# Performance work log

Hardware: AMD Instinct MI355X
Metric: run time of the kernel (lower is better)

Reference implementation:

```python
import jax, jax.numpy as jnp
import numpy as np

OBS_DIM = 4096
NUM_ACTIONS = 18
ACTION_DIM = 64
D_MODEL = 512
N_LAYERS = 4
HIST = 256
BATCH = 32
D_STATE = 16
D_CONV = 4
EXPAND = 2
D_INNER = EXPAND * D_MODEL           # 1024
DT_RANK = -(-D_MODEL // 16)          # ceil(512/16)=32
OBS_OUT = D_MODEL - ACTION_DIM       # 448


def setup_inputs() -> dict:
    key = jax.random.key(0)
    ks = jax.random.split(key, 16)
    s = 0.02
    inp = {
        "obss": jax.random.normal(ks[0], (BATCH, HIST, OBS_DIM), jnp.float32),
        "actions": jax.random.randint(ks[1], (BATCH, HIST, 1), 0, NUM_ACTIONS),
        "obs_W": jax.random.normal(ks[2], (OBS_OUT, OBS_DIM), jnp.float32) * s,
        "obs_b": jnp.zeros((OBS_OUT,), jnp.float32),
        "act_emb": jax.random.normal(ks[3], (NUM_ACTIONS, ACTION_DIM), jnp.float32) * s,
        "pos_emb": jax.random.normal(ks[4], (1, HIST, D_MODEL), jnp.float32) * s,
        # stacked Mamba params, leading dim = N_LAYERS
        "W_in": jax.random.normal(ks[5], (N_LAYERS, 2 * D_INNER, D_MODEL), jnp.float32) * s,
        "conv_w": jax.random.normal(ks[6], (N_LAYERS, D_INNER, D_CONV), jnp.float32) * s,
        "conv_b": jnp.zeros((N_LAYERS, D_INNER), jnp.float32),
        "W_x": jax.random.normal(ks[7], (N_LAYERS, DT_RANK + 2 * D_STATE, D_INNER), jnp.float32) * s,
        "W_dt": jax.random.normal(ks[8], (N_LAYERS, D_INNER, DT_RANK), jnp.float32) * s,
        "b_dt": jnp.full((N_LAYERS, D_INNER), -4.6, jnp.float32),  # softplus(-4.6)~0.01
        "A_log": jnp.log(jnp.broadcast_to(jnp.arange(1, D_STATE + 1, dtype=jnp.float32), (N_LAYERS, D_INNER, D_STATE))),
        "D_p": jnp.ones((N_LAYERS, D_INNER), jnp.float32),
        "W_out": jax.random.normal(ks[9], (N_LAYERS, D_MODEL, D_INNER), jnp.float32) * s,
        "ffn_W1": jax.random.normal(ks[10], (D_MODEL, D_MODEL), jnp.float32) * s,
        "ffn_b1": jnp.zeros((D_MODEL,), jnp.float32),
        "ffn_W2": jax.random.normal(ks[11], (NUM_ACTIONS, D_MODEL), jnp.float32) * s,
        "ffn_b2": jnp.zeros((NUM_ACTIONS,), jnp.float32),
    }
    return inp


def mamba_block(x, W_in, conv_w, conv_b, W_x, W_dt, b_dt, A_log, D_p, W_out):
    # x: (B, L, D_MODEL)
    B_, L, _ = x.shape
    xz = jnp.einsum('bld,ed->ble', x, W_in)            # (B,L,2*Di)
    xi, z = jnp.split(xz, 2, axis=-1)
    # causal depthwise conv1d, kernel D_CONV
    xp = jnp.pad(xi, ((0, 0), (D_CONV - 1, 0), (0, 0)))
    xc = conv_b + sum(conv_w[:, k] * xp[:, k:k + L, :] for k in range(D_CONV))
    xc = jax.nn.silu(xc)                               # (B,L,Di)
    xdbl = jnp.einsum('bld,ed->ble', xc, W_x)          # (B,L,dt_rank+2*ds)
    dt, Bm, Cm = jnp.split(xdbl, [DT_RANK, DT_RANK + D_STATE], axis=-1)
    dt = jax.nn.softplus(jnp.einsum('blr,dr->bld', dt, W_dt) + b_dt)  # (B,L,Di)
    A = -jnp.exp(A_log)                                # (Di,ds)

    def step(h, inp):
        dt_t, B_t, C_t, x_t = inp                      # (B,Di),(B,ds),(B,ds),(B,Di)
        dA = jnp.exp(dt_t[:, :, None] * A)             # (B,Di,ds)
        h = dA * h + dt_t[:, :, None] * B_t[:, None, :] * x_t[:, :, None]
        y = jnp.einsum('bdn,bn->bd', h, C_t)
        return h, y

    h0 = jnp.zeros((B_, D_INNER, D_STATE), xc.dtype)
    xs = (dt.transpose(1, 0, 2), Bm.transpose(1, 0, 2),
          Cm.transpose(1, 0, 2), xc.transpose(1, 0, 2))
    _, ys = jax.lax.scan(step, h0, xs)                 # (L,B,Di)
    y = ys.transpose(1, 0, 2) + xc * D_p
    y = y * jax.nn.silu(z)
    return jnp.einsum('bld,ed->ble', y, W_out)         # (B,L,D_MODEL)


def reference(obss, actions, obs_W, obs_b, act_emb, pos_emb, W_in, conv_w, conv_b,
              W_x, W_dt, b_dt, A_log, D_p, W_out, ffn_W1, ffn_b1, ffn_W2, ffn_b2):
    L = obss.shape[1]
    tok = jnp.einsum('blo,eo->ble', obss, obs_W) + obs_b          # (B,L,448)
    ae = act_emb[actions[:, :, 0]]                                # (B,L,64)
    # torch.roll(ae, 1, 1) with first step zeroed (history_len > 1)
    ae = jnp.concatenate([jnp.zeros_like(ae[:, :1]), ae[:, :-1]], axis=1)
    x = jnp.concatenate([ae, tok], axis=-1) + pos_emb[:, :L, :]   # (B,L,512)
    for i in range(N_LAYERS):
        x = mamba_block(x, W_in[i], conv_w[i], conv_b[i], W_x[i], W_dt[i],
                        b_dt[i], A_log[i], D_p[i], W_out[i])
    h = jax.nn.relu(jnp.einsum('bld,ed->ble', x, ffn_W1) + ffn_b1)
    out = jnp.einsum('bld,ed->ble', h, ffn_W2) + ffn_b2           # (B,L,18)
    return out[:, -L:, :]
```

## Files before the change

### kernel.cpp

```cpp
#include <hip/hip_runtime.h>
#include <hip/hip_bf16.h>
#include <cstdint>
#include <cstddef>

#define HIST    256
#define DMODEL  512
#define DINNER  1024
#define DSTATE  16
#define DTRANK  32
#define OBSDIM  4096
#define OBSOUT  448
#define ADIM    64
#define NLAYERS 4
#define MROWS   8192

typedef __bf16  bf16x8 __attribute__((ext_vector_type(8)));
typedef float   f32x4  __attribute__((ext_vector_type(4)));

enum { MEPI_TOK = 0, MEPI_BF16 = 1, MEPI_SPLIT = 2, MEPI_RELUB = 3, MEPI_PART = 4 };

__device__ __forceinline__ float siluf(float x) { return x / (1.f + __expf(-x)); }
__device__ __forceinline__ float softplusf(float x) {
    return fmaxf(x, 0.f) + log1pf(__expf(-fabsf(x)));
}
__device__ __forceinline__ float bflo(unsigned u) { return __uint_as_float(u << 16); }
__device__ __forceinline__ float bfhi(unsigned u) { return __uint_as_float(u & 0xffff0000u); }

template<int EPI, int NW>
__global__ __launch_bounds__(256)
void gemm_mfma(const __hip_bfloat16* __restrict__ A, int lda,
               const __hip_bfloat16* __restrict__ W,
               float* __restrict__ Cf, int ldc,
               __hip_bfloat16* __restrict__ Cb, int ldcb,
               int coff, int N, int K, int nbn,
               const float* __restrict__ bias, const float* __restrict__ pos)
{
    constexpr int MI   = (NW == 128) ? 4 : 2;
    constexpr int NBUF = (NW == 128) ? 3 : 4;
    __shared__ __hip_bfloat16 Asm[NBUF][128 * 32];
    __shared__ __hip_bfloat16 Bsm[NBUF][NW * 32];
    const int bid = blockIdx.x;
    const int xcd = bid & 7;
    const int s   = bid >> 3;
    int n_blk, m_blk, kc_ = 0;
    if constexpr (EPI == MEPI_PART) {
        m_blk = xcd * 8 + (s >> 2);
        kc_   = s & 3;
        n_blk = 0;
    } else {
        n_blk = s % nbn;
        m_blk = xcd * ((int)(gridDim.x >> 3) / nbn) + s / nbn;
    }
    const int m0 = m_blk * 128;
    const int n0 = n_blk * NW;

    const int tid  = threadIdx.x;
    const int lane = tid & 63;
    const int wv   = tid >> 6;
    const int wm   = (NW == 128) ? ((wv >> 1) << 6) : (wv << 5);
    const int wn   = (NW == 128) ? ((wv & 1) << 6) : 0;
    const int sr   = lane >> 2;
    const int scs  = (((lane & 3) ^ ((lane >> 4) & 3)) << 3);
    const int quad = lane >> 4;
    const int c16  = lane & 15;

    f32x4 acc[MI][4] = {};
    const __hip_bfloat16* aptr = A + (size_t)(m0 + wv * 16 + sr) * lda + scs + kc_ * 256;
    const __hip_bfloat16* bptr = W + (size_t)(n0 + wv * 16 + sr) * K + scs;

#define STAGE(K0, BUF) { \
    __hip_bfloat16* asml = Asm[BUF] + wv * 16 * 32; \
    __hip_bfloat16* bsml = Bsm[BUF] + wv * 16 * 32; \
    __builtin_amdgcn_global_load_lds( \
        (const __attribute__((address_space(1))) void*)(aptr + (K0)), \
        (__attribute__((address_space(3))) void*)(asml), 16, 0, 0); \
    __builtin_amdgcn_global_load_lds( \
        (const __attribute__((address_space(1))) void*)(aptr + (size_t)64 * lda + (K0)), \
        (__attribute__((address_space(3))) void*)(asml + 64 * 32), 16, 0, 0); \
    __builtin_amdgcn_global_load_lds( \
        (const __attribute__((address_space(1))) void*)(bptr + (K0)), \
        (__attribute__((address_space(3))) void*)(bsml), 16, 0, 0); \
    if (NW == 128) \
        __builtin_amdgcn_global_load_lds( \
            (const __attribute__((address_space(1))) void*)(bptr + (size_t)64 * K + (K0)), \
            (__attribute__((address_space(3))) void*)(bsml + 64 * 32), 16, 0, 0); \
    }

    auto kstep = [&](int buf) {
        __builtin_amdgcn_s_barrier();
        __builtin_amdgcn_sched_barrier(0);
        bf16x8 af[MI], bfr[4];
        const int csw = ((quad ^ ((c16 >> 2) & 3)) << 3);
        #pragma unroll
        for (int i = 0; i < MI; ++i)
            af[i]  = *(const bf16x8*)(Asm[buf] + (wm + i * 16 + c16) * 32 + csw);
        #pragma unroll
        for (int j = 0; j < 4; ++j)
            bfr[j] = *(const bf16x8*)(Bsm[buf] + (wn + j * 16 + c16) * 32 + csw);
        #pragma unroll
        for (int i = 0; i < MI; ++i)
            #pragma unroll
            for (int j = 0; j < 4; ++j)
                acc[i][j] = __builtin_amdgcn_mfma_f32_16x16x32_bf16(af[i], bfr[j], acc[i][j], 0, 0, 0);
        __builtin_amdgcn_sched_barrier(0);
        __builtin_amdgcn_s_barrier();
    };

    const int NT = K >> 5;
    #pragma unroll
    for (int t = 0; t < NBUF - 1; ++t) STAGE(t << 5, t)
    int sb = NBUF - 1, cb = 0;
    int it = 0;
    for (; it + NBUF - 1 < NT; ++it) {
        STAGE((it + NBUF - 1) << 5, sb)
        sb = (sb + 1 == NBUF) ? 0 : sb + 1;
        if constexpr (NW == 128) asm volatile("s_waitcnt vmcnt(8)" ::: "memory");
        else                     asm volatile("s_waitcnt vmcnt(9)" ::: "memory");
        kstep(cb);
        cb = (cb + 1 == NBUF) ? 0 : cb + 1;
    }
    if constexpr (NW == 64) {
        asm volatile("s_waitcnt vmcnt(6)" ::: "memory");
        kstep(cb); cb = (cb + 1 == NBUF) ? 0 : cb + 1;
        asm volatile("s_waitcnt vmcnt(3)" ::: "memory");
        kstep(cb); cb = (cb + 1 == NBUF) ? 0 : cb + 1;
        asm volatile("s_waitcnt vmcnt(0)" ::: "memory");
        kstep(cb);
    } else {
        asm volatile("s_waitcnt vmcnt(4)" ::: "memory");
        kstep(cb); cb = (cb + 1 == NBUF) ? 0 : cb + 1;
        asm volatile("s_waitcnt vmcnt(0)" ::: "memory");
        kstep(cb);
    }
#undef STAGE

    #pragma unroll
    for (int i = 0; i < MI; ++i) {
        const int mbase = m0 + wm + i * 16 + quad * 4;
        #pragma unroll
        for (int j = 0; j < 4; ++j) {
            const int n = n0 + wn + j * 16 + c16;
            if (n < N) {
                #pragma unroll
                for (int r = 0; r < 4; ++r) {
                    const size_t m = mbase + r;
                    float v = acc[i][j][r];
                    if (EPI == MEPI_TOK) {
                        v += bias[n] + pos[(m & (HIST - 1)) * DMODEL + coff + n];
                        Cb[m * ldcb + coff + n] = __float2bfloat16(v);
                    } else if (EPI == MEPI_BF16) {
                        Cb[m * ldcb + n] = __float2bfloat16(v);
                    } else if (EPI == MEPI_SPLIT) {
                        if (n < DTRANK) Cf[m * 32 + n] = v;
                        else Cb[(m >> 1) * 64 + (n & 15) * 4 + (m & 1) * 2 + ((n >> 4) & 1)]
                                 = __float2bfloat16(v);
                    } else if (EPI == MEPI_PART) {
                        Cf[((size_t)kc_ * MROWS + m) * 64 + n] = v;
                    } else {
                        Cb[m * ldcb + n] = __float2bfloat16(fmaxf(v + bias[n], 0.f));
                    }
                }
            }
        }
    }
}

__global__ __launch_bounds__(256)
void combine_split_kernel(const float* __restrict__ p, float* __restrict__ xdt,
                          __hip_bfloat16* __restrict__ bcb)
{
    const int idx = blockIdx.x * 256 + threadIdx.x;
    const int m  = idx >> 4;
    const int n4 = (idx & 15) << 2;
    const float4 a = *(const float4*)(p + (size_t)m * 64 + n4);
    const float4 b = *(const float4*)(p + ((size_t)MROWS + m) * 64 + n4);
    const float4 c = *(const float4*)(p + ((size_t)2 * MROWS + m) * 64 + n4);
    const float4 d = *(const float4*)(p + ((size_t)3 * MROWS + m) * 64 + n4);
    const float v[4] = { a.x + b.x + c.x + d.x, a.y + b.y + c.y + d.y,
                         a.z + b.z + c.z + d.z, a.w + b.w + c.w + d.w };
    if (n4 < 32) {
        *(float4*)(xdt + (size_t)m * 32 + n4) = make_float4(v[0], v[1], v[2], v[3]);
    } else {
        #pragma unroll
        for (int j = 0; j < 4; ++j) {
            const int n = n4 + j;
            bcb[(m >> 1) * 64 + (n & 15) * 4 + (m & 1) * 2 + ((n >> 4) & 1)]
                = __float2bfloat16(v[j]);
        }
    }
}

__global__ __launch_bounds__(256)
void gemm_f32_sp(const float* __restrict__ A, int lda,
                 const float* __restrict__ W,
                 __hip_bfloat16* __restrict__ C, int ldc,
                 int N, int K, const float* __restrict__ bias)
{
    __shared__ float As[32][68];
    __shared__ float Ws[32][68];
    const int tid = threadIdx.x;
    const int tx = tid & 15, ty = tid >> 4;
    const int m0 = blockIdx.y * 64;
    const int n0 = blockIdx.x * 64;
    const int lr = tid >> 3;
    const int lc = (tid & 7) << 2;
    float acc[4][4] = {};
    for (int k0 = 0; k0 < K; k0 += 32) {
        const float4 a0 = *(const float4*)(A + (size_t)(m0 + lr) * lda + k0 + lc);
        const float4 a1 = *(const float4*)(A + (size_t)(m0 + lr + 32) * lda + k0 + lc);
        const float4 b0 = *(const float4*)(W + (size_t)(n0 + lr) * K + k0 + lc);
        const float4 b1 = *(const float4*)(W + (size_t)(n0 + lr + 32) * K + k0 + lc);
        __syncthreads();
        As[lc+0][lr] = a0.x; As[lc+1][lr] = a0.y; As[lc+2][lr] = a0.z; As[lc+3][lr] = a0.w;
        As[lc+0][lr+32] = a1.x; As[lc+1][lr+32] = a1.y; As[lc+2][lr+32] = a1.z; As[lc+3][lr+32] = a1.w;
        Ws[lc+0][lr] = b0.x; Ws[lc+1][lr] = b0.y; Ws[lc+2][lr] = b0.z; Ws[lc+3][lr] = b0.w;
        Ws[lc+0][lr+32] = b1.x; Ws[lc+1][lr+32] = b1.y; Ws[lc+2][lr+32] = b1.z; Ws[lc+3][lr+32] = b1.w;
        __syncthreads();
        #pragma unroll
        for (int k = 0; k < 32; ++k) {
            const float4 a4 = *(const float4*)&As[k][ty << 2];
            const float4 b4 = *(const float4*)&Ws[k][tx << 2];
            const float a[4] = {a4.x, a4.y, a4.z, a4.w};
            const float b[4] = {b4.x, b4.y, b4.z, b4.w};
            #pragma unroll
            for (int i = 0; i < 4; ++i)
                #pragma unroll
                for (int j = 0; j < 4; ++j)
                    acc[i][j] = fmaf(a[i], b[j], acc[i][j]);
        }
    }
    const int mb = m0 + (ty << 2);
    const int nb = n0 + (tx << 2);
    #pragma unroll
    for (int i = 0; i < 4; ++i) {
        const size_t m = mb + i;
        #pragma unroll
        for (int j = 0; j < 4; ++j) {
            const int n = nb + j;
            C[m * ldc + n] = __float2bfloat16(softplusf(acc[i][j] + bias[n]));
        }
    }
}

#define NSEG 15
struct CastSegs {
    const float* src[NSEG];
    unsigned long long dstoff[NSEG];
    int blk_start[NSEG + 1];
    int n4[NSEG];
    int shift[NSEG];
    int nrows[NSEG];
};

__global__ __launch_bounds__(256)
void cast_all_kernel(CastSegs cs, char* wsbase)
{
    const int blk = blockIdx.x;
    int s = 0;
    #pragma unroll 1
    while (s < NSEG - 1 && blk >= cs.blk_start[s + 1]) ++s;
    const int i = (blk - cs.blk_start[s]) * 256 + (int)threadIdx.x;
    if (i >= cs.n4[s]) return;
    const int row = i >> cs.shift[s];
    float4 v = make_float4(0.f, 0.f, 0.f, 0.f);
    if (row < cs.nrows[s]) v = ((const float4*)cs.src[s])[i];
    union { __hip_bfloat16 h[4]; short4 sh; } o;
    o.h[0] = __float2bfloat16(v.x); o.h[1] = __float2bfloat16(v.y);
    o.h[2] = __float2bfloat16(v.z); o.h[3] = __float2bfloat16(v.w);
    ((short4*)(wsbase + cs.dstoff[s]))[i] = o.sh;
}

__global__ __launch_bounds__(256)
void embed_kernel(const int* __restrict__ actions, const float* __restrict__ act_emb,
                  const float* __restrict__ pos_emb, __hip_bfloat16* __restrict__ xb)
{
    const int idx = blockIdx.x * 256 + threadIdx.x;
    const int e = idx & 63;
    const int m = idx >> 6;
    const int l = m & (HIST - 1);
    const int b = m >> 8;
    float v = pos_emb[l * DMODEL + e];
    if (l > 0) {
        const int a = actions[b * HIST + l - 1];
        v += act_emb[a * ADIM + e];
    }
    xb[(size_t)m * DMODEL + e] = __float2bfloat16(v);
}

__global__ __launch_bounds__(256)
void conv_silu_kernel(const __hip_bfloat16* __restrict__ xzb, const float* __restrict__ cw,
                      const float* __restrict__ cb, __hip_bfloat16* __restrict__ xcb)
{
    const int idx = blockIdx.x * 256 + threadIdx.x;
    const int d = idx & (DINNER - 1);
    const int m = idx >> 10;
    const int l = m & (HIST - 1);
    const float4 w = ((const float4*)cw)[d];
    const __hip_bfloat16* basep = xzb + (size_t)m * (2 * DINNER) + d;
    float acc = cb[d] + w.w * __bfloat162float(basep[0]);
    if (l >= 1) acc = fmaf(w.z, __bfloat162float(basep[-2 * DINNER]), acc);
    if (l >= 2) acc = fmaf(w.y, __bfloat162float(basep[-4 * DINNER]), acc);
    if (l >= 3) acc = fmaf(w.x, __bfloat162float(basep[-6 * DINNER]), acc);
    xcb[idx] = __float2bfloat16(siluf(acc));
}

#define DPPA(x, CTRL) { float _t; \
    asm("v_add_f32_dpp %0, %1, %1 " CTRL " row_mask:0xf bank_mask:0xf" \
        : "=v"(_t) : "v"(x)); x = _t; }

__global__ __launch_bounds__(256)
void scan_kernel(const __hip_bfloat16* __restrict__ dtb, const __hip_bfloat16* __restrict__ bcb,
                 const __hip_bfloat16* __restrict__ xcb, const __hip_bfloat16* __restrict__ zb,
                 const float* __restrict__ A_log, const float* __restrict__ D_p,
                 __hip_bfloat16* __restrict__ yb)
{
    __shared__ unsigned sdx[2][16][68];
    __shared__ unsigned sbc[2][16][68];

    const int tid = threadIdx.x;
    const int n   = tid & 15;
    const int g   = tid >> 4;

    const int bid = blockIdx.x;
    const int blk = ((bid & 7) << 8) | (bid >> 3);
    const int c0  = blk * 16;
    const int b   = c0 >> 10;
    const int d0  = c0 & (DINNER - 1);
    const int d   = d0 + g;
    const size_t row0 = (size_t)b * HIST;

    const int sr = tid >> 2;
    const int sq = tid & 3;
    const unsigned short* dtu = (const unsigned short*)dtb;
    const unsigned short* xcu = (const unsigned short*)xcb;
    const unsigned short* zu  = (const unsigned short*)zb;
    const unsigned*       bcu = (const unsigned*)bcb;

    const float Ar = -__expf(A_log[d * DSTATE + n]);
#if __has_builtin(__builtin_amdgcn_exp2f)
    const float A2 = Ar * 1.44269504089f;
#define DAEXP(x) __builtin_amdgcn_exp2f((x) * A2)
#else
#define DAEXP(x) __expf((x) * Ar)
#endif
    const float Dp = D_p[d];
    float h = 0.f;

    uint2 dv, xv; uint4 bv;
    unsigned short za[4], znx[4];

#define SLOAD(cc) { \
    const size_t rb = (row0 + (size_t)(cc) * 64 + sr) * DINNER + d0 + sq * 4; \
    dv = *(const uint2*)(dtu + rb); \
    xv = *(const uint2*)(xcu + rb); \
    bv = *(const uint4*)(bcu + row0 * 16 + (size_t)(cc) * 1024 + tid * 4); \
}
#define SWRITE(bb) { \
    const int ch = sq * 4; \
    sdx[bb][ch + 0][sr] = (dv.x & 0xffffu) | (xv.x << 16); \
    sdx[bb][ch + 1][sr] = (dv.x >> 16)     | (xv.x & 0xffff0000u); \
    sdx[bb][ch + 2][sr] = (dv.y & 0xffffu) | (xv.y << 16); \
    sdx[bb][ch + 3][sr] = (dv.y >> 16)     | (xv.y & 0xffff0000u); \
    const int e2 = (tid & 7) * 2, p2 = (tid >> 3) * 2; \
    sbc[bb][e2 + 0][p2 + 0] = bv.x; \
    sbc[bb][e2 + 0][p2 + 1] = bv.y; \
    sbc[bb][e2 + 1][p2 + 0] = bv.z; \
    sbc[bb][e2 + 1][p2 + 1] = bv.w; \
}
#define ZLOAD(cc, arr) { \
    _Pragma("unroll") \
    for (int w = 0; w < 4; ++w) \
        arr[w] = zu[(row0 + (size_t)(cc) * 64 + w * 16 + n) * (2 * DINNER) + d0 + g]; \
}
#define SSTEP(Q, R, KK) { \
    const float dt = bflo(Q), xc = bfhi(Q); \
    const float Bv = bflo(R), Cv = bfhi(R); \
    const float dA = DAEXP(dt); \
    h = fmaf(dA, h, dt * xc * Bv); \
    float ctr = h * Cv; \
    DPPA(ctr, "quad_perm:[1,0,3,2]") \
    DPPA(ctr, "quad_perm:[2,3,0,1]") \
    DPPA(ctr, "row_half_mirror") \
    DPPA(ctr, "row_mirror") \
    if (n == (KK)) yreg = ctr; \
}

    SLOAD(0)
    ZLOAD(0, za)
    SWRITE(0)
    __syncthreads();

    for (int c = 0; c < 4; ++c) {
        const int buf = c & 1;
        if (c < 3) { SLOAD(c + 1) ZLOAD(c + 1, znx) }

        const unsigned (*sdxc)[68] = sdx[buf];
        const unsigned (*sbcc)[68] = sbc[buf];
        #pragma unroll
        for (int w = 0; w < 4; ++w) {
            float yreg = 0.f;
            #pragma unroll
            for (int jq = 0; jq < 4; ++jq) {
                const uint4 qv = *(const uint4*)&sdxc[g][w * 16 + jq * 4];
                const uint4 rv = *(const uint4*)&sbcc[n][w * 16 + jq * 4];
                SSTEP(qv.x, rv.x, jq * 4 + 0)
                SSTEP(qv.y, rv.y, jq * 4 + 1)
                SSTEP(qv.z, rv.z, jq * 4 + 2)
                SSTEP(qv.w, rv.w, jq * 4 + 3)
            }
            const float xcf = bfhi(sdxc[g][w * 16 + n]);
            const float ze  = __uint_as_float((unsigned)za[w] << 16);
            yb[(row0 + c * 64 + w * 16 + n) * DINNER + d] =
                __float2bfloat16((yreg + xcf * Dp) * siluf(ze));
        }

        if (c < 3) SWRITE((c + 1) & 1)
        __syncthreads();
        #pragma unroll
        for (int w = 0; w < 4; ++w) za[w] = znx[w];
    }
#undef SLOAD
#undef SWRITE
#undef ZLOAD
#undef SSTEP
#undef DAEXP
}

__global__ __launch_bounds__(256)
void ffn2_kernel(const __hip_bfloat16* __restrict__ h, const float* __restrict__ W2,
                 const float* __restrict__ b2, float* __restrict__ out)
{
    const int idx = blockIdx.x * 256 + threadIdx.x;
    const int n = idx & 31;
    const int m = idx >> 5;
    if (n >= 18) return;
    const unsigned short* hr = (const unsigned short*)(h + (size_t)m * DMODEL);
    const float* wr = W2 + (size_t)n * DMODEL;
    float acc = b2[n];
    for (int k = 0; k < DMODEL; k += 8) {
        const uint4 hv = *(const uint4*)(hr + k);
        const float4 w0 = *(const float4*)(wr + k);
        const float4 w1 = *(const float4*)(wr + k + 4);
        acc = fmaf(bflo(hv.x), w0.x, acc);
        acc = fmaf(bfhi(hv.x), w0.y, acc);
        acc = fmaf(bflo(hv.y), w0.z, acc);
        acc = fmaf(bfhi(hv.y), w0.w, acc);
        acc = fmaf(bflo(hv.z), w1.x, acc);
        acc = fmaf(bfhi(hv.z), w1.y, acc);
        acc = fmaf(bflo(hv.w), w1.z, acc);
        acc = fmaf(bfhi(hv.w), w1.w, acc);
    }
    out[(size_t)m * 18 + n] = acc;
}

extern "C" void kernel_launch(void* const* d_in, const int* in_sizes, int n_in,
                              void* d_out, int out_size, void* d_ws, size_t ws_size,
                              hipStream_t stream)
{
    const float* obss    = (const float*)d_in[0];
    const int*   actions = (const int*)  d_in[1];
    const float* obs_W   = (const float*)d_in[2];
    const float* obs_b   = (const float*)d_in[3];
    const float* act_emb = (const float*)d_in[4];
    const float* pos_emb = (const float*)d_in[5];
    const float* W_in    = (const float*)d_in[6];
    const float* conv_w  = (const float*)d_in[7];
    const float* conv_b  = (const float*)d_in[8];
    const float* W_x     = (const float*)d_in[9];
    const float* W_dt    = (const float*)d_in[10];
    const float* b_dt    = (const float*)d_in[11];
    const float* A_log   = (const float*)d_in[12];
    const float* D_p     = (const float*)d_in[13];
    const float* W_out   = (const float*)d_in[14];
    const float* ffn_W1  = (const float*)d_in[15];
    const float* ffn_b1  = (const float*)d_in[16];
    const float* ffn_W2  = (const float*)d_in[17];
    const float* ffn_b2  = (const float*)d_in[18];
    float* out = (float*)d_out;

    const size_t MiB = 1024 * 1024;
    char* base = (char*)d_ws;
    __hip_bfloat16* xb    = (__hip_bfloat16*)(base);
    __hip_bfloat16* xzb   = (__hip_bfloat16*)(base + 8 * MiB);
    __hip_bfloat16* xcb   = (__hip_bfloat16*)(base + 40 * MiB);
    __hip_bfloat16* dtb   = (__hip_bfloat16*)(base + 56 * MiB);
    __hip_bfloat16* yb    = (__hip_bfloat16*)(base + 88 * MiB);
    float*          xdt   = (float*)(base + 104 * MiB);
    __hip_bfloat16* bcb   = (__hip_bfloat16*)(base + 105 * MiB);
    float*          xdtp  = (float*)(base + 112 * MiB);
    __hip_bfloat16* obssb = (__hip_bfloat16*)(base + 8 * MiB);
    __hip_bfloat16* hbuf  = (__hip_bfloat16*)(base + 8 * MiB);
    const size_t WOBS_OFF = 128 * MiB;
    const size_t WIN_OFF  = 132 * MiB;
    const size_t WOUT_OFF = 140 * MiB;
    const size_t WX_OFF   = 144 * MiB;
    const size_t WF1_OFF  = 145 * MiB;

    CastSegs cs{};
    int nb = 0, si = 0;
    auto addseg = [&](const float* src, size_t dstoff, int n4, int shift, int nrows) {
        cs.src[si] = src; cs.dstoff[si] = dstoff; cs.n4[si] = n4;
        cs.shift[si] = shift; cs.nrows[si] = nrows;
        cs.blk_start[si] = nb; nb += (n4 + 255) / 256; ++si;
    };
    addseg(obss, 8 * MiB, MROWS * OBSDIM / 4, 31, 0x7fffffff);
    addseg(obs_W, WOBS_OFF, 512 * (OBSDIM / 4), 10, OBSOUT);
    for (int i = 0; i < NLAYERS; ++i)
        addseg(W_in + (size_t)i * 2 * DINNER * DMODEL, WIN_OFF + (size_t)i * 2 * MiB,
               2 * DINNER * DMODEL / 4, 31, 0x7fffffff);
    for (int i = 0; i < NLAYERS; ++i)
        addseg(W_out + (size_t)i * DMODEL * DINNER, WOUT_OFF + (size_t)i * MiB,
               DMODEL * DINNER / 4, 31, 0x7fffffff);
    for (int i = 0; i < NLAYERS; ++i)
        addseg(W_x + (size_t)i * 64 * DINNER, WX_OFF + (size_t)i * (MiB / 4),
               128 * (DINNER / 4), 8, 64);
    addseg(ffn_W1, WF1_OFF, DMODEL * DMODEL / 4, 31, 0x7fffffff);
    cs.blk_start[si] = nb;
    cast_all_kernel<<<nb, 256, 0, stream>>>(cs, (char*)d_ws);

    embed_kernel<<<MROWS * ADIM / 256, 256, 0, stream>>>(actions, act_emb, pos_emb, xb);
    gemm_mfma<MEPI_TOK, 64><<<8 * (MROWS / 128), 256, 0, stream>>>(
        obssb, OBSDIM, (__hip_bfloat16*)(base + WOBS_OFF), nullptr, 0, xb, DMODEL,
        ADIM, OBSOUT, OBSDIM, 8, obs_b, pos_emb);

    for (int i = 0; i < NLAYERS; ++i) {
        gemm_mfma<MEPI_BF16, 128><<<(2 * DINNER / 128) * (MROWS / 128), 256, 0, stream>>>(
            xb, DMODEL, (__hip_bfloat16*)(base + WIN_OFF + (size_t)i * 2 * MiB),
            nullptr, 0, xzb, 2 * DINNER, 0, 2 * DINNER, DMODEL,
            2 * DINNER / 128, nullptr, nullptr);
        conv_silu_kernel<<<MROWS * DINNER / 256, 256, 0, stream>>>(
            xzb, conv_w + (size_t)i * DINNER * 4, conv_b + (size_t)i * DINNER, xcb);
        gemm_mfma<MEPI_PART, 64><<<256, 256, 0, stream>>>(
            xcb, DINNER, (__hip_bfloat16*)(base + WX_OFF + (size_t)i * (MiB / 4)),
            xdtp, 0, nullptr, 0, 0, 64, 256, 1, nullptr, nullptr);
        combine_split_kernel<<<MROWS * 16 / 256, 256, 0, stream>>>(xdtp, xdt, bcb);
        gemm_f32_sp<<<dim3(DINNER / 64, MROWS / 64), 256, 0, stream>>>(
            xdt, 32, W_dt + (size_t)i * DINNER * DTRANK, dtb, DINNER, DINNER, DTRANK,
            b_dt + (size_t)i * DINNER);
        scan_kernel<<<(32 * DINNER) / 16, 256, 0, stream>>>(
            dtb, bcb, xcb, xzb + DINNER, A_log + (size_t)i * DINNER * DSTATE,
            D_p + (size_t)i * DINNER, yb);
        gemm_mfma<MEPI_BF16, 64><<<(DMODEL / 64) * (MROWS / 128), 256, 0, stream>>>(
            yb, DINNER, (__hip_bfloat16*)(base + WOUT_OFF + (size_t)i * MiB),
            nullptr, 0, xb, DMODEL, 0, DMODEL, DINNER,
            DMODEL / 64, nullptr, nullptr);
    }

    gemm_mfma<MEPI_RELUB, 64><<<(DMODEL / 64) * (MROWS / 128), 256, 0, stream>>>(
        xb, DMODEL, (__hip_bfloat16*)(base + WF1_OFF), nullptr, 0, hbuf, DMODEL,
        0, DMODEL, DMODEL, DMODEL / 64, ffn_b1, nullptr);
    ffn2_kernel<<<MROWS * 32 / 256, 256, 0, stream>>>(hbuf, ffn_W2, ffn_b2, out);
}
```

Before: 1.108 ms.

## Split-K the observation projection GEMM with 128-wide tiles and separate combine

The obs-token GEMM (K=4096) now runs on 128x128 tiles with a split-K of 2 across 512 blocks. Fp32 partials go to a workspace, and a new combine kernel adds bias and positional embedding, converts to bf16 and writes into the token buffer. The cast kernel also becomes a grid-stride loop over a fixed grid instead of one block per 256 float4s. This is meant to raise MFMA efficiency and parallelism for the largest GEMM. In exchange it adds an extra kernel launch and an fp32 partial write and read round trip of about 32 MB.

```diff
diff --git a/kernel.cpp b/kernel.cpp
--- a/kernel.cpp
+++ b/kernel.cpp
@@ -17,7 +17,7 @@
 typedef __bf16  bf16x8 __attribute__((ext_vector_type(8)));
 typedef float   f32x4  __attribute__((ext_vector_type(4)));
 
-enum { MEPI_TOK = 0, MEPI_BF16 = 1, MEPI_SPLIT = 2, MEPI_RELUB = 3, MEPI_PART = 4 };
+enum { MEPI_TOK = 0, MEPI_BF16 = 1, MEPI_SPLIT = 2, MEPI_RELUB = 3, MEPI_PART = 4, MEPI_PTOK = 5 };
 
 __device__ __forceinline__ float siluf(float x) { return x / (1.f + __expf(-x)); }
 __device__ __forceinline__ float softplusf(float x) {
@@ -32,7 +32,7 @@
                const __hip_bfloat16* __restrict__ W,
                float* __restrict__ Cf, int ldc,
                __hip_bfloat16* __restrict__ Cb, int ldcb,
-               int coff, int N, int K, int nbn,
+               int coff, int N, int K, int wld, int nbn,
                const float* __restrict__ bias, const float* __restrict__ pos)
 {
     constexpr int MI   = (NW == 128) ? 4 : 2;
@@ -47,12 +47,17 @@
         m_blk = xcd * 8 + (s >> 2);
         kc_   = s & 3;
         n_blk = 0;
+    } else if constexpr (EPI == MEPI_PTOK) {
+        m_blk = xcd * 8 + (s >> 3);
+        n_blk = (s >> 1) & 3;
+        kc_   = s & 1;
     } else {
         n_blk = s % nbn;
         m_blk = xcd * ((int)(gridDim.x >> 3) / nbn) + s / nbn;
     }
     const int m0 = m_blk * 128;
     const int n0 = n_blk * NW;
+    const int kch = (EPI == MEPI_PART) ? kc_ * 256 : (EPI == MEPI_PTOK) ? kc_ * 2048 : 0;
 
     const int tid  = threadIdx.x;
     const int lane = tid & 63;
@@ -65,8 +70,8 @@
     const int c16  = lane & 15;
 
     f32x4 acc[MI][4] = {};
-    const __hip_bfloat16* aptr = A + (size_t)(m0 + wv * 16 + sr) * lda + scs + kc_ * 256;
-    const __hip_bfloat16* bptr = W + (size_t)(n0 + wv * 16 + sr) * K + scs;
+    const __hip_bfloat16* aptr = A + (size_t)(m0 + wv * 16 + sr) * lda + scs + kch;
+    const __hip_bfloat16* bptr = W + (size_t)(n0 + wv * 16 + sr) * wld + scs + kch;
 
 #define STAGE(K0, BUF) { \
     __hip_bfloat16* asml = Asm[BUF] + wv * 16 * 32; \
@@ -82,7 +87,7 @@
         (__attribute__((address_space(3))) void*)(bsml), 16, 0, 0); \
     if (NW == 128) \
         __builtin_amdgcn_global_load_lds( \
-            (const __attribute__((address_space(1))) void*)(bptr + (size_t)64 * K + (K0)), \
+            (const __attribute__((address_space(1))) void*)(bptr + (size_t)64 * wld + (K0)), \
             (__attribute__((address_space(3))) void*)(bsml + 64 * 32), 16, 0, 0); \
     }
 
@@ -145,10 +150,7 @@
                 for (int r = 0; r < 4; ++r) {
                     const size_t m = mbase + r;
                     float v = acc[i][j][r];
-                    if (EPI == MEPI_TOK) {
-                        v += bias[n] + pos[(m & (HIST - 1)) * DMODEL + coff + n];
-                        Cb[m * ldcb + coff + n] = __float2bfloat16(v);
-                    } else if (EPI == MEPI_BF16) {
+                    if (EPI == MEPI_BF16) {
                         Cb[m * ldcb + n] = __float2bfloat16(v);
                     } else if (EPI == MEPI_SPLIT) {
                         if (n < DTRANK) Cf[m * 32 + n] = v;
@@ -156,6 +158,8 @@
                                  = __float2bfloat16(v);
                     } else if (EPI == MEPI_PART) {
                         Cf[((size_t)kc_ * MROWS + m) * 64 + n] = v;
+                    } else if (EPI == MEPI_PTOK) {
+                        Cf[((size_t)kc_ * MROWS + m) * 512 + n] = v;
                     } else {
                         Cb[m * ldcb + n] = __float2bfloat16(fmaxf(v + bias[n], 0.f));
                     }
@@ -187,6 +191,29 @@
             bcb[(m >> 1) * 64 + (n & 15) * 4 + (m & 1) * 2 + ((n >> 4) & 1)]
                 = __float2bfloat16(v[j]);
         }
+    }
+}
+
+__global__ __launch_bounds__(256)
+void combine_tok_kernel(const float* __restrict__ p, const float* __restrict__ bias,
+                        const float* __restrict__ pos, __hip_bfloat16* __restrict__ xb)
+{
+    const int stride = gridDim.x * 256;
+    const int TOT = MROWS * (OBSOUT / 4);
+    for (int g = blockIdx.x * 256 + (int)threadIdx.x; g < TOT; g += stride) {
+        const int m  = g / (OBSOUT / 4);
+        const int n4 = (g - m * (OBSOUT / 4)) * 4;
+        const float4 a  = *(const float4*)(p + (size_t)m * 512 + n4);
+        const float4 b  = *(const float4*)(p + ((size_t)MROWS + m) * 512 + n4);
+        const int l = m & (HIST - 1);
+        const float4 bs = *(const float4*)(bias + n4);
+        const float4 ps = *(const float4*)(pos + (size_t)l * DMODEL + ADIM + n4);
+        union { __hip_bfloat16 h[4]; short4 s; } o;
+        o.h[0] = __float2bfloat16(a.x + b.x + bs.x + ps.x);
+        o.h[1] = __float2bfloat16(a.y + b.y + bs.y + ps.y);
+        o.h[2] = __float2bfloat16(a.z + b.z + bs.z + ps.z);
+        o.h[3] = __float2bfloat16(a.w + b.w + bs.w + ps.w);
+        *(short4*)(xb + (size_t)m * DMODEL + ADIM + n4) = o.s;
     }
 }
 
@@ -246,28 +273,28 @@
 struct CastSegs {
     const float* src[NSEG];
     unsigned long long dstoff[NSEG];
-    int blk_start[NSEG + 1];
-    int n4[NSEG];
+    int el_start[NSEG + 1];
     int shift[NSEG];
     int nrows[NSEG];
 };
 
 __global__ __launch_bounds__(256)
-void cast_all_kernel(CastSegs cs, char* wsbase)
-{
-    const int blk = blockIdx.x;
-    int s = 0;
-    #pragma unroll 1
-    while (s < NSEG - 1 && blk >= cs.blk_start[s + 1]) ++s;
-    const int i = (blk - cs.blk_start[s]) * 256 + (int)threadIdx.x;
-    if (i >= cs.n4[s]) return;
-    const int row = i >> cs.shift[s];
-    float4 v = make_float4(0.f, 0.f, 0.f, 0.f);
-    if (row < cs.nrows[s]) v = ((const float4*)cs.src[s])[i];
-    union { __hip_bfloat16 h[4]; short4 sh; } o;
-    o.h[0] = __float2bfloat16(v.x); o.h[1] = __float2bfloat16(v.y);
-    o.h[2] = __float2bfloat16(v.z); o.h[3] = __float2bfloat16(v.w);
-    ((short4*)(wsbase + cs.dstoff[s]))[i] = o.sh;
+void cast_all_kernel(CastSegs cs, char* wsbase, int total4)
+{
+    const int stride = gridDim.x * 256;
+    for (int g = blockIdx.x * 256 + (int)threadIdx.x; g < total4; g += stride) {
+        int s = 0;
+        #pragma unroll 1
+        while (s < NSEG - 1 && g >= cs.el_start[s + 1]) ++s;
+        const int i = g - cs.el_start[s];
+        const int row = i >> cs.shift[s];
+        float4 v = make_float4(0.f, 0.f, 0.f, 0.f);
+        if (row < cs.nrows[s]) v = ((const float4*)cs.src[s])[i];
+        union { __hip_bfloat16 h[4]; short4 sh; } o;
+        o.h[0] = __float2bfloat16(v.x); o.h[1] = __float2bfloat16(v.y);
+        o.h[2] = __float2bfloat16(v.z); o.h[3] = __float2bfloat16(v.w);
+        ((short4*)(wsbase + cs.dstoff[s]))[i] = o.sh;
+    }
 }
 
 __global__ __launch_bounds__(256)
@@ -495,13 +522,14 @@
     const size_t WOUT_OFF = 140 * MiB;
     const size_t WX_OFF   = 144 * MiB;
     const size_t WF1_OFF  = 145 * MiB;
+    float*          tokp  = (float*)(base + 160 * MiB);
 
     CastSegs cs{};
-    int nb = 0, si = 0;
+    int nel = 0, si = 0;
     auto addseg = [&](const float* src, size_t dstoff, int n4, int shift, int nrows) {
-        cs.src[si] = src; cs.dstoff[si] = dstoff; cs.n4[si] = n4;
+        cs.src[si] = src; cs.dstoff[si] = dstoff;
         cs.shift[si] = shift; cs.nrows[si] = nrows;
-        cs.blk_start[si] = nb; nb += (n4 + 255) / 256; ++si;
+        cs.el_start[si] = nel; nel += n4; ++si;
     };
     addseg(obss, 8 * MiB, MROWS * OBSDIM / 4, 31, 0x7fffffff);
     addseg(obs_W, WOBS_OFF, 512 * (OBSDIM / 4), 10, OBSOUT);
@@ -515,24 +543,25 @@
         addseg(W_x + (size_t)i * 64 * DINNER, WX_OFF + (size_t)i * (MiB / 4),
                128 * (DINNER / 4), 8, 64);
     addseg(ffn_W1, WF1_OFF, DMODEL * DMODEL / 4, 31, 0x7fffffff);
-    cs.blk_start[si] = nb;
-    cast_all_kernel<<<nb, 256, 0, stream>>>(cs, (char*)d_ws);
+    cs.el_start[si] = nel;
+    cast_all_kernel<<<2048, 256, 0, stream>>>(cs, (char*)d_ws, nel);
 
     embed_kernel<<<MROWS * ADIM / 256, 256, 0, stream>>>(actions, act_emb, pos_emb, xb);
-    gemm_mfma<MEPI_TOK, 64><<<8 * (MROWS / 128), 256, 0, stream>>>(
-        obssb, OBSDIM, (__hip_bfloat16*)(base + WOBS_OFF), nullptr, 0, xb, DMODEL,
-        ADIM, OBSOUT, OBSDIM, 8, obs_b, pos_emb);
+    gemm_mfma<MEPI_PTOK, 128><<<512, 256, 0, stream>>>(
+        obssb, OBSDIM, (const __hip_bfloat16*)(base + WOBS_OFF), tokp, 0, nullptr, 0,
+        0, 512, 2048, OBSDIM, 1, nullptr, nullptr);
+    combine_tok_kernel<<<1024, 256, 0, stream>>>(tokp, obs_b, pos_emb, xb);
 
     for (int i = 0; i < NLAYERS; ++i) {
         gemm_mfma<MEPI_BF16, 128><<<(2 * DINNER / 128) * (MROWS / 128), 256, 0, stream>>>(
-            xb, DMODEL, (__hip_bfloat16*)(base + WIN_OFF + (size_t)i * 2 * MiB),
-            nullptr, 0, xzb, 2 * DINNER, 0, 2 * DINNER, DMODEL,
+            xb, DMODEL, (const __hip_bfloat16*)(base + WIN_OFF + (size_t)i * 2 * MiB),
+            nullptr, 0, xzb, 2 * DINNER, 0, 2 * DINNER, DMODEL, DMODEL,
             2 * DINNER / 128, nullptr, nullptr);
         conv_silu_kernel<<<MROWS * DINNER / 256, 256, 0, stream>>>(
             xzb, conv_w + (size_t)i * DINNER * 4, conv_b + (size_t)i * DINNER, xcb);
         gemm_mfma<MEPI_PART, 64><<<256, 256, 0, stream>>>(
-            xcb, DINNER, (__hip_bfloat16*)(base + WX_OFF + (size_t)i * (MiB / 4)),
-            xdtp, 0, nullptr, 0, 0, 64, 256, 1, nullptr, nullptr);
+            xcb, DINNER, (const __hip_bfloat16*)(base + WX_OFF + (size_t)i * (MiB / 4)),
+            xdtp, 0, nullptr, 0, 0, 64, 256, DINNER, 1, nullptr, nullptr);
         combine_split_kernel<<<MROWS * 16 / 256, 256, 0, stream>>>(xdtp, xdt, bcb);
         gemm_f32_sp<<<dim3(DINNER / 64, MROWS / 64), 256, 0, stream>>>(
             xdt, 32, W_dt + (size_t)i * DINNER * DTRANK, dtb, DINNER, DINNER, DTRANK,
@@ -541,13 +570,13 @@
             dtb, bcb, xcb, xzb + DINNER, A_log + (size_t)i * DINNER * DSTATE,
             D_p + (size_t)i * DINNER, yb);
         gemm_mfma<MEPI_BF16, 64><<<(DMODEL / 64) * (MROWS / 128), 256, 0, stream>>>(
-            yb, DINNER, (__hip_bfloat16*)(base + WOUT_OFF + (size_t)i * MiB),
-            nullptr, 0, xb, DMODEL, 0, DMODEL, DINNER,
+            yb, DINNER, (const __hip_bfloat16*)(base + WOUT_OFF + (size_t)i * MiB),
+            nullptr, 0, xb, DMODEL, 0, DMODEL, DINNER, DINNER,
             DMODEL / 64, nullptr, nullptr);
     }
 
     gemm_mfma<MEPI_RELUB, 64><<<(DMODEL / 64) * (MROWS / 128), 256, 0, stream>>>(
-        xb, DMODEL, (__hip_bfloat16*)(base + WF1_OFF), nullptr, 0, hbuf, DMODEL,
-        0, DMODEL, DMODEL, DMODEL / 64, ffn_b1, nullptr);
+        xb, DMODEL, (const __hip_bfloat16*)(base + WF1_OFF), nullptr, 0, hbuf, DMODEL,
+        0, DMODEL, DMODEL, DMODEL, DMODEL / 64, ffn_b1, nullptr);
     ffn2_kernel<<<MROWS * 32 / 256, 256, 0, stream>>>(hbuf, ffn_W2, ffn_b2, out);
 }
```

Result: no change. 1.102 ms (-0.6%).
